# Performance work log

Measured on AMD Instinct MI355X. Metric: run time of the kernel, lower is better.

The kernel has to match this reference:

```python
import jax, jax.numpy as jnp
import numpy as np

N, E, B, K = 100000, 3200000, 500, 30
F_IN, H1, NUM_CLASSES = 128, 64, 18


def _gcn_conv(x, W, b, row, col, w_edge, n_nodes):
    # PyG GCNConv: remove_self_loops happened outside (w_edge=0 on self loops),
    # GCNConv re-adds self loops -> deg = in_deg + 1, norm = d^-1/2[row]*d^-1/2[col].
    xw = x @ W
    deg = jax.ops.segment_sum(w_edge, col, num_segments=n_nodes) + 1.0
    dis = jax.lax.rsqrt(deg)
    coef = dis[row] * dis[col] * w_edge           # [E]
    msg = xw[row] * coef[:, None]                 # [E, C] irregular gather
    agg = jax.ops.segment_sum(msg, col, num_segments=n_nodes)
    agg = agg + xw * (dis * dis)[:, None]         # self-loop term
    return agg + b


def _sort_pool(x, batch, num_graphs, k):
    # SortAggregation: per-graph sort descending by last channel, keep top-k, zero-pad.
    n, c = x.shape
    score = x[:, -1]
    perm = jnp.lexsort((-score, batch))           # sort by (batch asc, score desc)
    b_sorted = batch[perm]
    counts = jax.ops.segment_sum(jnp.ones((n,), x.dtype), batch, num_segments=num_graphs)
    starts = jnp.cumsum(counts) - counts          # segment start offsets
    pos = jnp.arange(n) - starts[b_sorted].astype(jnp.int32)
    pos = jnp.where(pos < k, pos, k)              # out-of-range -> dropped
    out = jnp.zeros((num_graphs, k, c), x.dtype).at[b_sorted, pos].set(x[perm], mode='drop')
    return out.reshape(num_graphs, k * c)


def _conv1d(x, w, b, stride):
    y = jax.lax.conv_general_dilated(x, w, (stride,), 'VALID',
                                     dimension_numbers=('NCH', 'OIH', 'NCH'))
    return y + b[None, :, None]


def setup_inputs() -> dict:
    key = jax.random.key(0)
    ks = jax.random.split(key, 16)
    x = jax.random.normal(ks[0], (N, F_IN), dtype=jnp.float32)
    edge_index = jax.random.randint(ks[1], (2, E), 0, N, dtype=jnp.int32)
    batch = jnp.sort(jax.random.randint(ks[2], (N,), 0, B, dtype=jnp.int32))
    s = 0.05
    return {
        'x': x, 'edge_index': edge_index, 'batch': batch, 'num_graphs': B,
        'W1': jax.random.normal(ks[3], (F_IN, H1), jnp.float32) * s,
        'b1': jnp.zeros((H1,), jnp.float32),
        'W2': jax.random.normal(ks[4], (H1, 1), jnp.float32) * s,
        'b2': jnp.zeros((1,), jnp.float32),
        'conv3_w': jax.random.normal(ks[5], (16, 1, 97), jnp.float32) * s,
        'conv3_b': jnp.zeros((16,), jnp.float32),
        'conv4_w': jax.random.normal(ks[6], (32, 16, 5), jnp.float32) * s,
        'conv4_b': jnp.zeros((32,), jnp.float32),
        'fc1_w': jax.random.normal(ks[7], (192, 128), jnp.float32) * s,
        'fc1_b': jnp.zeros((128,), jnp.float32),
        'fc2_w': jax.random.normal(ks[8], (128, NUM_CLASSES), jnp.float32) * s,
        'fc2_b': jnp.zeros((NUM_CLASSES,), jnp.float32),
    }


def reference(x, edge_index, batch, num_graphs, W1, b1, W2, b2,
              conv3_w, conv3_b, conv4_w, conv4_b, fc1_w, fc1_b, fc2_w, fc2_b):
    row, col = edge_index[0], edge_index[1]
    w_edge = (row != col).astype(x.dtype)         # remove_self_loops
    x1 = jnp.tanh(_gcn_conv(x, W1, b1, row, col, w_edge, x.shape[0]))   # [N,64]
    x2 = jnp.tanh(_gcn_conv(x1, W2, b2, row, col, w_edge, x.shape[0]))  # [N,1]
    xc = jnp.concatenate([x1, x2], axis=-1)       # [N,65]
    p = _sort_pool(xc, batch, num_graphs, K)      # [B, 1950]
    h = p[:, None, :]                             # [B,1,1950]
    h = jax.nn.relu(_conv1d(h, conv3_w, conv3_b, 97))                   # [B,16,20]
    h = jax.lax.reduce_window(h, -jnp.inf, jax.lax.max,
                              (1, 1, 2), (1, 1, 2), 'VALID')            # [B,16,10]
    h = jax.nn.relu(_conv1d(h, conv4_w, conv4_b, 1))                    # [B,32,6]
    h = h.reshape(h.shape[0], -1)                 # [B,192]
    last_layer = jax.nn.relu(h @ fc1_w + fc1_b)   # [B,128] (dropout = eval identity)
    out = last_layer @ fc2_w + fc2_b              # [B,18]
    classes = jax.nn.log_softmax(out, axis=-1)
    return (classes, out, last_layer)
```

## Files before the change

### kernel.cpp

```cpp
#include <hip/hip_runtime.h>
#include <math.h>

#define N_NODES 100000
#define N_EDGES 3200000
#define B_GRAPHS 500
#define K_TOP 30
#define F_INN 128
#define H1C 64
#define NUM_CLASSES 18
#define XC 65
#define P_LEN (K_TOP * XC)
#define C3_OUT 16
#define C3_K 97
#define C3_L 20
#define P2_L 10
#define C4_OUT 32
#define C4_K 5
#define C4_L 6
#define FC1_IN 192
#define FC1_OUT 128

#define BK_SHIFT 7
#define BK_NODES 128
#define NBKT ((N_NODES + BK_NODES - 1) / BK_NODES)
#define BSTRIDE 5120
#define MS_EPT 16
#define MS_EPB (256 * MS_EPT)

typedef __attribute__((ext_vector_type(8))) short bf16x8;
typedef __attribute__((ext_vector_type(4))) float f32x4;

static __device__ __forceinline__ unsigned short f2bf(float f) {
    unsigned int u = __float_as_uint(f);
    u += 0x7FFFu + ((u >> 16) & 1u);
    return (unsigned short)(u >> 16);
}
static __device__ __forceinline__ float bfl(unsigned int u) {
    return __uint_as_float(u << 16);
}
static __device__ __forceinline__ float bfh(unsigned int u) {
    return __uint_as_float(u & 0xFFFF0000u);
}

__global__ __launch_bounds__(256) void k_mscatter(const int* __restrict__ row,
                                                  const int* __restrict__ col,
                                                  int* __restrict__ gcur,
                                                  unsigned int* __restrict__ ebkt) {
    __shared__ int hist[NBKT];
    __shared__ int base[NBKT];
    int tid = threadIdx.x;
    for (int i = tid; i < NBKT; i += 256) hist[i] = 0;
    __syncthreads();
    unsigned int pk[MS_EPT];
    unsigned int pay[MS_EPT];
    int e0 = blockIdx.x * MS_EPB;
#pragma unroll
    for (int j = 0; j < MS_EPT; ++j) {
        int e = e0 + j * 256 + tid;
        pk[j] = 0xFFFFFFFFu;
        if (e < N_EDGES) {
            int r = row[e], c = col[e];
            if (r != c) {
                int b = c >> BK_SHIFT;
                int rank = atomicAdd(&hist[b], 1);
                pk[j] = ((unsigned int)b << 12) | (unsigned int)rank;
                pay[j] = ((unsigned int)r << BK_SHIFT) | (unsigned int)(c & (BK_NODES - 1));
            }
        }
    }
    __syncthreads();
    for (int i = tid; i < NBKT; i += 256)
        base[i] = hist[i] ? (i * BSTRIDE + atomicAdd(&gcur[i], hist[i])) : 0;
    __syncthreads();
#pragma unroll
    for (int j = 0; j < MS_EPT; ++j) {
        if (pk[j] != 0xFFFFFFFFu) {
            int b = pk[j] >> 12;
            int rank = pk[j] & 0xFFF;
            ebkt[base[b] + rank] = pay[j];
        }
    }
}

__global__ __launch_bounds__(256) void k_csr(const unsigned int* __restrict__ ebkt,
                                             const int* __restrict__ gcur,
                                             float* __restrict__ dis,
                                             int2* __restrict__ rowse,
                                             int* __restrict__ erow) {
    __shared__ int cnt[BK_NODES];
    __shared__ int s[256];
    __shared__ int cur[BK_NODES];
    int b = blockIdx.x, t = threadIdx.x;
    if (t < BK_NODES) cnt[t] = 0;
    __syncthreads();
    int lo = b * BSTRIDE;
    int hi = lo + gcur[b];
    for (int i = lo + t; i < hi; i += 256)
        atomicAdd(&cnt[ebkt[i] & (BK_NODES - 1)], 1);
    __syncthreads();
    int v = (t < BK_NODES) ? cnt[t] : 0;
    s[t] = v;
    __syncthreads();
    for (int off = 1; off < BK_NODES; off <<= 1) {
        int add = (t >= off) ? s[t - off] : 0;
        __syncthreads();
        s[t] += add;
        __syncthreads();
    }
    int ex = s[t] - v;
    if (t < BK_NODES) {
        int node = b * BK_NODES + t;
        if (node < N_NODES) {
            dis[node] = rsqrtf((float)v + 1.0f);
            rowse[node] = make_int2(lo + ex, lo + ex + v);
        }
        cur[t] = lo + ex;
    }
    __syncthreads();
    for (int i = lo + t; i < hi; i += 256) {
        unsigned int pk = ebkt[i];
        int cl = pk & (BK_NODES - 1);
        int slot = atomicAdd(&cur[cl], 1);
        erow[slot] = (int)((pk >> BK_SHIFT) << 7);
    }
}

__global__ __launch_bounds__(256) void k_xw1(const float* __restrict__ x,
                                             const float* __restrict__ W1,
                                             const float* __restrict__ dis,
                                             unsigned short* __restrict__ xw) {
    __shared__ unsigned short w1s[16 * 64 * 8];
    int tid = threadIdx.x;
    if (blockIdx.x == 0 && tid < 32)
        ((unsigned int*)(xw + (size_t)N_NODES * H1C))[tid] = 0;
    for (int idx = tid; idx < 16 * 64 * 8; idx += 256) {
        int f = idx >> 9;
        int l = (idx >> 3) & 63;
        int j = idx & 7;
        int kq = f >> 2, t4 = f & 3;
        int k = kq * 32 + ((l >> 4) << 3) + j;
        int n = t4 * 16 + (l & 15);
        w1s[idx] = f2bf(W1[k * H1C + n]);
    }
    __syncthreads();
    int wave = tid >> 6;
    int lane = tid & 63;
    int quad = lane >> 4;
    int m = lane & 15;
    int wrow0 = blockIdx.x * 64 + wave * 16;

    bf16x8 bw[16];
#pragma unroll
    for (int f = 0; f < 16; ++f)
        bw[f] = *(const bf16x8*)&w1s[(f * 64 + lane) * 8];

    f32x4 acc[4];
#pragma unroll
    for (int t = 0; t < 4; ++t) acc[t] = (f32x4){0.f, 0.f, 0.f, 0.f};

    int rowA = wrow0 + m;
    size_t ra = (size_t)(rowA < N_NODES ? rowA : N_NODES - 1);
#pragma unroll
    for (int kq = 0; kq < 4; ++kq) {
        const float* xp = x + ra * F_INN + kq * 32 + quad * 8;
        float4 f0 = ((const float4*)xp)[0];
        float4 f1 = ((const float4*)xp)[1];
        bf16x8 a;
        a[0] = (short)f2bf(f0.x); a[1] = (short)f2bf(f0.y);
        a[2] = (short)f2bf(f0.z); a[3] = (short)f2bf(f0.w);
        a[4] = (short)f2bf(f1.x); a[5] = (short)f2bf(f1.y);
        a[6] = (short)f2bf(f1.z); a[7] = (short)f2bf(f1.w);
#pragma unroll
        for (int t = 0; t < 4; ++t)
            acc[t] = __builtin_amdgcn_mfma_f32_16x16x32_bf16(a, bw[kq * 4 + t], acc[t], 0, 0, 0);
    }
#pragma unroll
    for (int r = 0; r < 4; ++r) {
        int rowD = wrow0 + quad * 4 + r;
        if (rowD < N_NODES) {
            float dsc = dis[rowD];
#pragma unroll
            for (int t = 0; t < 4; ++t)
                xw[(size_t)rowD * H1C + t * 16 + m] = f2bf(acc[t][r] * dsc);
        }
    }
}

__global__ __launch_bounds__(256) void k_agg1f(const int2* __restrict__ rowse,
                                               const int* __restrict__ erow,
                                               const unsigned short* __restrict__ xws,
                                               const float* __restrict__ dis,
                                               const float* __restrict__ b1,
                                               const float* __restrict__ W2,
                                               float* __restrict__ x1,
                                               float* __restrict__ xws2) {
    __shared__ float accs[4][64];
    int tid = threadIdx.x;
    int wave = tid >> 6;
    int lane = tid & 63;
    int wid = blockIdx.x * 4 + wave;
    int grp = lane >> 3;
    int sub = lane & 7;
    int2 se = rowse[wid];
    int base = se.x, endp = se.y;
    const char* xb = (const char*)xws;
    const int ZR = N_NODES << 7;
    float acc[8] = {0.f, 0.f, 0.f, 0.f, 0.f, 0.f, 0.f, 0.f};
    for (int e0 = base; e0 < endp; e0 += 16) {
        int i0 = e0 + grp;
        int i1 = e0 + 8 + grp;
        int o0 = (i0 < endp) ? erow[i0] : ZR;
        int o1 = (i1 < endp) ? erow[i1] : ZR;
        uint4 a = ((const uint4*)(xb + o0))[sub];
        uint4 bq = ((const uint4*)(xb + o1))[sub];
        acc[0] += bfl(a.x) + bfl(bq.x);
        acc[1] += bfh(a.x) + bfh(bq.x);
        acc[2] += bfl(a.y) + bfl(bq.y);
        acc[3] += bfh(a.y) + bfh(bq.y);
        acc[4] += bfl(a.z) + bfl(bq.z);
        acc[5] += bfh(a.z) + bfh(bq.z);
        acc[6] += bfl(a.w) + bfl(bq.w);
        acc[7] += bfh(a.w) + bfh(bq.w);
    }
#pragma unroll
    for (int i = 0; i < 8; ++i) {
        acc[i] += __shfl_xor(acc[i], 8);
        acc[i] += __shfl_xor(acc[i], 16);
        acc[i] += __shfl_xor(acc[i], 32);
    }
    if (grp == 0) {
#pragma unroll
        for (int i = 0; i < 8; ++i) accs[wave][sub * 8 + i] = acc[i];
    }
    __syncthreads();
    float d = dis[wid];
    unsigned int su = xws[(size_t)wid * H1C + lane];
    float self = __uint_as_float(su << 16);
    float v = tanhf(d * (accs[wave][lane] + self) + b1[lane]);
    x1[(size_t)wid * H1C + lane] = v;
    float s = v * W2[lane];
#pragma unroll
    for (int off = 1; off < 64; off <<= 1) s += __shfl_xor(s, off);
    if (lane == 0) xws2[wid] = d * s;
}

__global__ __launch_bounds__(256) void k_x2(const int2* __restrict__ rowse,
                                            const int* __restrict__ erow,
                                            const float* __restrict__ xws2,
                                            const float* __restrict__ dis,
                                            const float* __restrict__ b2,
                                            float* __restrict__ x2) {
    int lane = threadIdx.x & 63;
    int wglob = (blockIdx.x * 256 + threadIdx.x) >> 6;
    int grp = lane >> 3;
    int sub = lane & 7;
    int node = wglob * 8 + grp;
    int2 se = rowse[node];
    float acc = 0.0f;
    for (int i = se.x + sub; i < se.y; i += 8)
        acc += xws2[erow[i] >> 7];
    acc += __shfl_xor(acc, 1);
    acc += __shfl_xor(acc, 2);
    acc += __shfl_xor(acc, 4);
    if (sub == 0)
        x2[node] = tanhf(dis[node] * (acc + xws2[node]) + b2[0]);
}

__global__ __launch_bounds__(256) void k_poolhead(const int* __restrict__ batch,
                                                  const float* __restrict__ x1,
                                                  const float* __restrict__ x2,
                                                  const float* __restrict__ w3, const float* __restrict__ b3,
                                                  const float* __restrict__ w4, const float* __restrict__ b4,
                                                  const float* __restrict__ fw1, const float* __restrict__ fb1,
                                                  const float* __restrict__ fw2, const float* __restrict__ fb2,
                                                  float* __restrict__ out) {
    __shared__ float x2s[512];
    __shared__ int sel[K_TOP];
    __shared__ float ps[P_LEN];
    __shared__ float h1s[C3_OUT * C3_L];
    __shared__ float h2s[C3_OUT * P2_L];
    __shared__ float h3s[FC1_IN];
    __shared__ float lls[FC1_OUT];
    __shared__ float outs[NUM_CLASSES];
    int g = blockIdx.x, tid = threadIdx.x;
    int lo = 0, hi = N_NODES;
    while (lo < hi) { int m = (lo + hi) >> 1; if (batch[m] < g) lo = m + 1; else hi = m; }
    int start = lo;
    hi = N_NODES;
    while (lo < hi) { int m = (lo + hi) >> 1; if (batch[m] < g + 1) lo = m + 1; else hi = m; }
    int end = lo;
    int count = end - start;
    if (count > 512) count = 512;
    for (int t = tid; t < count; t += 256) x2s[t] = x2[start + t];
    __syncthreads();
    int wave = tid >> 6, lane = tid & 63;
    if (wave == 0) {
        unsigned long long k[8];
#pragma unroll
        for (int i = 0; i < 8; ++i) {
            int idx = i * 64 + lane;
            unsigned long long key = 0ULL;
            if (idx < count) {
                unsigned int bits = __float_as_uint(x2s[idx]);
                unsigned int u = (bits & 0x80000000u) ? ~bits : (bits | 0x80000000u);
                key = ((unsigned long long)u << 32) | (unsigned int)(~(unsigned int)(start + idx));
            }
            k[i] = key;
        }
        int kk = count < K_TOP ? count : K_TOP;
        for (int j = 0; j < kk; ++j) {
            unsigned long long best = k[0];
#pragma unroll
            for (int i = 1; i < 8; ++i) if (k[i] > best) best = k[i];
#pragma unroll
            for (int off = 32; off; off >>= 1) {
                unsigned long long o = __shfl_xor(best, off);
                if (o > best) best = o;
            }
            int node = (int)(~(unsigned int)(best & 0xFFFFFFFFULL));
#pragma unroll
            for (int i = 0; i < 8; ++i) if (k[i] == best) k[i] = 0ULL;
            if (lane == 0) sel[j] = node;
        }
        if (lane >= kk && lane < K_TOP) sel[lane] = -1;
    }
    __syncthreads();
    for (int t = tid; t < P_LEN; t += 256) {
        int j = t / XC, c = t - j * XC;
        int node = sel[j];
        float v = 0.0f;
        if (node >= 0) v = (c < H1C) ? x1[(size_t)node * H1C + c] : x2s[node - start];
        ps[t] = v;
    }
    __syncthreads();
    for (int o = tid; o < C3_OUT * C3_L; o += 256) {
        int oc = o / C3_L, pos = o % C3_L;
        float s = b3[oc];
        const float* w = w3 + oc * C3_K;
        int base = pos * C3_K;
        for (int k = 0; k < C3_K; ++k) s += ps[base + k] * w[k];
        h1s[o] = fmaxf(s, 0.0f);
    }
    __syncthreads();
    if (tid < C3_OUT * P2_L) {
        int oc = tid / P2_L, pos = tid % P2_L;
        h2s[tid] = fmaxf(h1s[oc * C3_L + 2 * pos], h1s[oc * C3_L + 2 * pos + 1]);
    }
    __syncthreads();
    if (tid < C4_OUT * C4_L) {
        int oc = tid / C4_L, pos = tid % C4_L;
        float s = b4[oc];
        for (int ic = 0; ic < C3_OUT; ++ic)
#pragma unroll
            for (int k = 0; k < C4_K; ++k)
                s += h2s[ic * P2_L + pos + k] * w4[oc * C3_OUT * C4_K + ic * C4_K + k];
        h3s[oc * C4_L + pos] = fmaxf(s, 0.0f);
    }
    __syncthreads();
    if (tid < FC1_OUT) {
        float s = fb1[tid];
        for (int i = 0; i < FC1_IN; ++i) s += h3s[i] * fw1[i * FC1_OUT + tid];
        float v = fmaxf(s, 0.0f);
        lls[tid] = v;
        out[2 * B_GRAPHS * NUM_CLASSES + (size_t)g * FC1_OUT + tid] = v;
    }
    __syncthreads();
    if (tid < NUM_CLASSES) {
        float s = fb2[tid];
        for (int j = 0; j < FC1_OUT; ++j) s += lls[j] * fw2[j * NUM_CLASSES + tid];
        outs[tid] = s;
        out[B_GRAPHS * NUM_CLASSES + (size_t)g * NUM_CLASSES + tid] = s;
    }
    __syncthreads();
    if (tid < NUM_CLASSES) {
        float m = -INFINITY;
        for (int k2 = 0; k2 < NUM_CLASSES; ++k2) m = fmaxf(m, outs[k2]);
        float se = 0.0f;
        for (int k2 = 0; k2 < NUM_CLASSES; ++k2) se += expf(outs[k2] - m);
        out[(size_t)g * NUM_CLASSES + tid] = outs[tid] - m - logf(se);
    }
}

extern "C" void kernel_launch(void* const* d_in, const int* in_sizes, int n_in,
                              void* d_out, int out_size, void* d_ws, size_t ws_size,
                              hipStream_t stream) {
    const float* x   = (const float*)d_in[0];
    const int*   ei  = (const int*)d_in[1];
    const int*   row = ei;
    const int*   col = ei + N_EDGES;
    const int*   bat = (const int*)d_in[2];
    const float* W1  = (const float*)d_in[4];
    const float* b1  = (const float*)d_in[5];
    const float* W2  = (const float*)d_in[6];
    const float* b2  = (const float*)d_in[7];
    const float* w3  = (const float*)d_in[8];
    const float* b3  = (const float*)d_in[9];
    const float* w4  = (const float*)d_in[10];
    const float* b4  = (const float*)d_in[11];
    const float* fw1 = (const float*)d_in[12];
    const float* fb1 = (const float*)d_in[13];
    const float* fw2 = (const float*)d_in[14];
    const float* fb2 = (const float*)d_in[15];

    char* wsb = (char*)d_ws;
    unsigned short* xws = (unsigned short*)wsb;       wsb += (size_t)(N_NODES + 1) * H1C * 2;
    float* x1     = (float*)wsb;                      wsb += (size_t)N_NODES * H1C * 4;
    int*   erow   = (int*)wsb;                        wsb += (size_t)NBKT * BSTRIDE * 4;
    unsigned int* ebkt = (unsigned int*)x1;
    int*   gcur   = (int*)wsb;                        wsb += (size_t)NBKT * 4;
    int2*  rowse  = (int2*)wsb;                       wsb += (size_t)N_NODES * 8;
    float* dis    = (float*)wsb;                      wsb += (size_t)N_NODES * 4;
    float* xws2   = (float*)wsb;                      wsb += (size_t)N_NODES * 4;
    float* x2     = (float*)wsb;                      wsb += (size_t)N_NODES * 4;
    float* outp   = (float*)d_out;

    hipMemsetAsync(gcur, 0, (size_t)NBKT * 4, stream);

    k_mscatter<<<(N_EDGES + MS_EPB - 1) / MS_EPB, 256, 0, stream>>>(row, col, gcur, ebkt);
    k_csr<<<NBKT, 256, 0, stream>>>(ebkt, gcur, dis, rowse, erow);
    k_xw1<<<(N_NODES + 63) / 64, 256, 0, stream>>>(x, W1, dis, xws);
    k_agg1f<<<N_NODES / 4, 256, 0, stream>>>(rowse, erow, xws, dis, b1, W2, x1, xws2);
    k_x2<<<N_NODES / (8 * 4), 256, 0, stream>>>(rowse, erow, xws2, dis, b2, x2);
    k_poolhead<<<B_GRAPHS, 256, 0, stream>>>(bat, x1, x2,
                                             w3, b3, w4, b4, fw1, fb1, fw2, fb2, outp);
}
```

Measured before the change: 334.8 us.

## Build CSR with global per-node atomics and prefetch first 64 neighbors

Replaces the two-pass bucketed scatter plus per-bucket local CSR build with three kernels. The first counts in-degree per node with global atomics, the second computes per-node offsets inside fixed bucket strides, and the third scatters row indices straight into CSR slots through global atomic cursors. This drops the intermediate bucket array and its second pass, at the cost of many global atomics that contend on random destination nodes. The layer-1 aggregation now loads the first 64 neighbor offsets with one coalesced read, shuffles them across lanes and issues 8 independent gathers up front to raise memory-level parallelism. Edges beyond 64 fall back to a loop.

```diff
diff --git a/kernel.cpp b/kernel.cpp
--- a/kernel.cpp
+++ b/kernel.cpp
@@ -24,8 +24,6 @@
 #define BK_NODES 128
 #define NBKT ((N_NODES + BK_NODES - 1) / BK_NODES)
 #define BSTRIDE 5120
-#define MS_EPT 16
-#define MS_EPB (256 * MS_EPT)
 
 typedef __attribute__((ext_vector_type(8))) short bf16x8;
 typedef __attribute__((ext_vector_type(4))) float f32x4;
@@ -42,63 +40,26 @@
     return __uint_as_float(u & 0xFFFF0000u);
 }
 
-__global__ __launch_bounds__(256) void k_mscatter(const int* __restrict__ row,
-                                                  const int* __restrict__ col,
-                                                  int* __restrict__ gcur,
-                                                  unsigned int* __restrict__ ebkt) {
-    __shared__ int hist[NBKT];
-    __shared__ int base[NBKT];
-    int tid = threadIdx.x;
-    for (int i = tid; i < NBKT; i += 256) hist[i] = 0;
-    __syncthreads();
-    unsigned int pk[MS_EPT];
-    unsigned int pay[MS_EPT];
-    int e0 = blockIdx.x * MS_EPB;
-#pragma unroll
-    for (int j = 0; j < MS_EPT; ++j) {
-        int e = e0 + j * 256 + tid;
-        pk[j] = 0xFFFFFFFFu;
-        if (e < N_EDGES) {
-            int r = row[e], c = col[e];
-            if (r != c) {
-                int b = c >> BK_SHIFT;
-                int rank = atomicAdd(&hist[b], 1);
-                pk[j] = ((unsigned int)b << 12) | (unsigned int)rank;
-                pay[j] = ((unsigned int)r << BK_SHIFT) | (unsigned int)(c & (BK_NODES - 1));
-            }
-        }
-    }
-    __syncthreads();
-    for (int i = tid; i < NBKT; i += 256)
-        base[i] = hist[i] ? (i * BSTRIDE + atomicAdd(&gcur[i], hist[i])) : 0;
-    __syncthreads();
-#pragma unroll
-    for (int j = 0; j < MS_EPT; ++j) {
-        if (pk[j] != 0xFFFFFFFFu) {
-            int b = pk[j] >> 12;
-            int rank = pk[j] & 0xFFF;
-            ebkt[base[b] + rank] = pay[j];
-        }
-    }
-}
-
-__global__ __launch_bounds__(256) void k_csr(const unsigned int* __restrict__ ebkt,
-                                             const int* __restrict__ gcur,
-                                             float* __restrict__ dis,
-                                             int2* __restrict__ rowse,
-                                             int* __restrict__ erow) {
-    __shared__ int cnt[BK_NODES];
-    __shared__ int s[256];
-    __shared__ int cur[BK_NODES];
+__global__ __launch_bounds__(256) void k_count(const int* __restrict__ row,
+                                               const int* __restrict__ col,
+                                               int* __restrict__ ncnt) {
+    int t = blockIdx.x * 256 + threadIdx.x;
+    int4 r4 = ((const int4*)row)[t];
+    int4 c4 = ((const int4*)col)[t];
+    if (r4.x != c4.x) atomicAdd(&ncnt[c4.x], 1);
+    if (r4.y != c4.y) atomicAdd(&ncnt[c4.y], 1);
+    if (r4.z != c4.z) atomicAdd(&ncnt[c4.z], 1);
+    if (r4.w != c4.w) atomicAdd(&ncnt[c4.w], 1);
+}
+
+__global__ __launch_bounds__(128) void k_nodebase(const int* __restrict__ ncnt,
+                                                  float* __restrict__ dis,
+                                                  int2* __restrict__ rowse,
+                                                  int* __restrict__ cur) {
+    __shared__ int s[BK_NODES];
     int b = blockIdx.x, t = threadIdx.x;
-    if (t < BK_NODES) cnt[t] = 0;
-    __syncthreads();
-    int lo = b * BSTRIDE;
-    int hi = lo + gcur[b];
-    for (int i = lo + t; i < hi; i += 256)
-        atomicAdd(&cnt[ebkt[i] & (BK_NODES - 1)], 1);
-    __syncthreads();
-    int v = (t < BK_NODES) ? cnt[t] : 0;
+    int node = b * BK_NODES + t;
+    int v = (node < N_NODES) ? ncnt[node] : 0;
     s[t] = v;
     __syncthreads();
     for (int off = 1; off < BK_NODES; off <<= 1) {
@@ -108,21 +69,25 @@
         __syncthreads();
     }
     int ex = s[t] - v;
-    if (t < BK_NODES) {
-        int node = b * BK_NODES + t;
-        if (node < N_NODES) {
-            dis[node] = rsqrtf((float)v + 1.0f);
-            rowse[node] = make_int2(lo + ex, lo + ex + v);
-        }
-        cur[t] = lo + ex;
-    }
-    __syncthreads();
-    for (int i = lo + t; i < hi; i += 256) {
-        unsigned int pk = ebkt[i];
-        int cl = pk & (BK_NODES - 1);
-        int slot = atomicAdd(&cur[cl], 1);
-        erow[slot] = (int)((pk >> BK_SHIFT) << 7);
-    }
+    if (node < N_NODES) {
+        int base = b * BSTRIDE + ex;
+        dis[node] = rsqrtf((float)v + 1.0f);
+        rowse[node] = make_int2(base, base + v);
+        cur[node] = base;
+    }
+}
+
+__global__ __launch_bounds__(256) void k_scatter2(const int* __restrict__ row,
+                                                  const int* __restrict__ col,
+                                                  int* __restrict__ cur,
+                                                  int* __restrict__ erow) {
+    int t = blockIdx.x * 256 + threadIdx.x;
+    int4 r4 = ((const int4*)row)[t];
+    int4 c4 = ((const int4*)col)[t];
+    if (r4.x != c4.x) { int s = atomicAdd(&cur[c4.x], 1); erow[s] = r4.x << BK_SHIFT; }
+    if (r4.y != c4.y) { int s = atomicAdd(&cur[c4.y], 1); erow[s] = r4.y << BK_SHIFT; }
+    if (r4.z != c4.z) { int s = atomicAdd(&cur[c4.z], 1); erow[s] = r4.z << BK_SHIFT; }
+    if (r4.w != c4.w) { int s = atomicAdd(&cur[c4.w], 1); erow[s] = r4.w << BK_SHIFT; }
 }
 
 __global__ __launch_bounds__(256) void k_xw1(const float* __restrict__ x,
@@ -203,24 +168,40 @@
     int sub = lane & 7;
     int2 se = rowse[wid];
     int base = se.x, endp = se.y;
+    int nE = endp - base;
     const char* xb = (const char*)xws;
     const int ZR = N_NODES << 7;
+
+    int myoff = (lane < nE) ? erow[base + lane] : ZR;
+
+    uint4 a[8];
+#pragma unroll
+    for (int k = 0; k < 8; ++k) {
+        int o = __shfl(myoff, (k << 3) + grp);
+        a[k] = ((const uint4*)(xb + o))[sub];
+    }
     float acc[8] = {0.f, 0.f, 0.f, 0.f, 0.f, 0.f, 0.f, 0.f};
-    for (int e0 = base; e0 < endp; e0 += 16) {
-        int i0 = e0 + grp;
-        int i1 = e0 + 8 + grp;
-        int o0 = (i0 < endp) ? erow[i0] : ZR;
-        int o1 = (i1 < endp) ? erow[i1] : ZR;
-        uint4 a = ((const uint4*)(xb + o0))[sub];
-        uint4 bq = ((const uint4*)(xb + o1))[sub];
-        acc[0] += bfl(a.x) + bfl(bq.x);
-        acc[1] += bfh(a.x) + bfh(bq.x);
-        acc[2] += bfl(a.y) + bfl(bq.y);
-        acc[3] += bfh(a.y) + bfh(bq.y);
-        acc[4] += bfl(a.z) + bfl(bq.z);
-        acc[5] += bfh(a.z) + bfh(bq.z);
-        acc[6] += bfl(a.w) + bfl(bq.w);
-        acc[7] += bfh(a.w) + bfh(bq.w);
+#pragma unroll
+    for (int k = 0; k < 8; ++k) {
+        acc[0] += bfl(a[k].x);
+        acc[1] += bfh(a[k].x);
+        acc[2] += bfl(a[k].y);
+        acc[3] += bfh(a[k].y);
+        acc[4] += bfl(a[k].z);
+        acc[5] += bfh(a[k].z);
+        acc[6] += bfl(a[k].w);
+        acc[7] += bfh(a[k].w);
+    }
+    if (nE > 64) {
+        for (int e0 = base + 64; e0 < endp; e0 += 8) {
+            int i = e0 + grp;
+            int o = (i < endp) ? erow[i] : ZR;
+            uint4 q = ((const uint4*)(xb + o))[sub];
+            acc[0] += bfl(q.x); acc[1] += bfh(q.x);
+            acc[2] += bfl(q.y); acc[3] += bfh(q.y);
+            acc[4] += bfl(q.z); acc[5] += bfh(q.z);
+            acc[6] += bfl(q.w); acc[7] += bfh(q.w);
+        }
     }
 #pragma unroll
     for (int i = 0; i < 8; ++i) {
@@ -406,18 +387,19 @@
     unsigned short* xws = (unsigned short*)wsb;       wsb += (size_t)(N_NODES + 1) * H1C * 2;
     float* x1     = (float*)wsb;                      wsb += (size_t)N_NODES * H1C * 4;
     int*   erow   = (int*)wsb;                        wsb += (size_t)NBKT * BSTRIDE * 4;
-    unsigned int* ebkt = (unsigned int*)x1;
-    int*   gcur   = (int*)wsb;                        wsb += (size_t)NBKT * 4;
     int2*  rowse  = (int2*)wsb;                       wsb += (size_t)N_NODES * 8;
     float* dis    = (float*)wsb;                      wsb += (size_t)N_NODES * 4;
     float* xws2   = (float*)wsb;                      wsb += (size_t)N_NODES * 4;
     float* x2     = (float*)wsb;                      wsb += (size_t)N_NODES * 4;
-    float* outp   = (float*)d_out;
-
-    hipMemsetAsync(gcur, 0, (size_t)NBKT * 4, stream);
-
-    k_mscatter<<<(N_EDGES + MS_EPB - 1) / MS_EPB, 256, 0, stream>>>(row, col, gcur, ebkt);
-    k_csr<<<NBKT, 256, 0, stream>>>(ebkt, gcur, dis, rowse, erow);
+    int* ncnt = (int*)x1;
+    int* cur  = ncnt + N_NODES;
+    float* outp = (float*)d_out;
+
+    hipMemsetAsync(ncnt, 0, (size_t)N_NODES * 4, stream);
+
+    k_count<<<N_EDGES / 1024, 256, 0, stream>>>(row, col, ncnt);
+    k_nodebase<<<NBKT, 128, 0, stream>>>(ncnt, dis, rowse, cur);
+    k_scatter2<<<N_EDGES / 1024, 256, 0, stream>>>(row, col, cur, erow);
     k_xw1<<<(N_NODES + 63) / 64, 256, 0, stream>>>(x, W1, dis, xws);
     k_agg1f<<<N_NODES / 4, 256, 0, stream>>>(rowse, erow, xws, dis, b1, W2, x1, xws2);
     k_x2<<<N_NODES / (8 * 4), 256, 0, stream>>>(rowse, erow, xws2, dis, b2, x2);
```

After: 679.6 us. 2.03x slower.

## Sum gathered neighbor rows with MFMA via LDS transpose reads

Applied to the files above, without the earlier changes.

The per-node neighbor aggregation in the first GCN layer no longer accumulates bf16 values with scalar adds and shuffle reductions. Each wave stages gathered neighbor rows into LDS, reads them back transposed with ds_read_b64_tr_b16, and sums them by multiplying with an all-ones bf16 matrix on MFMA. This moves the accumulation to the matrix cores and drops the cross-lane reduction and block-wide barrier. In exchange it adds LDS round trips and explicit waitcnt stalls per 32 edges, and pads partial chunks with zero-row loads; the gather latency still dominates.

```diff
diff --git a/kernel.cpp b/kernel.cpp
--- a/kernel.cpp
+++ b/kernel.cpp
@@ -27,19 +27,16 @@
 #define MS_EPT 16
 #define MS_EPB (256 * MS_EPT)
 
+#define REG_B 544
+
 typedef __attribute__((ext_vector_type(8))) short bf16x8;
 typedef __attribute__((ext_vector_type(4))) float f32x4;
+typedef __attribute__((ext_vector_type(2))) unsigned int u32x2;
 
 static __device__ __forceinline__ unsigned short f2bf(float f) {
     unsigned int u = __float_as_uint(f);
     u += 0x7FFFu + ((u >> 16) & 1u);
     return (unsigned short)(u >> 16);
-}
-static __device__ __forceinline__ float bfl(unsigned int u) {
-    return __uint_as_float(u << 16);
-}
-static __device__ __forceinline__ float bfh(unsigned int u) {
-    return __uint_as_float(u & 0xFFFF0000u);
 }
 
 __global__ __launch_bounds__(256) void k_mscatter(const int* __restrict__ row,
@@ -186,7 +183,7 @@
     }
 }
 
-__global__ __launch_bounds__(256) void k_agg1f(const int2* __restrict__ rowse,
+__global__ __launch_bounds__(256) void k_agg1m(const int2* __restrict__ rowse,
                                                const int* __restrict__ erow,
                                                const unsigned short* __restrict__ xws,
                                                const float* __restrict__ dis,
@@ -194,7 +191,7 @@
                                                const float* __restrict__ W2,
                                                float* __restrict__ x1,
                                                float* __restrict__ xws2) {
-    __shared__ float accs[4][64];
+    __shared__ __align__(16) char slds[4][8 * REG_B];
     int tid = threadIdx.x;
     int wave = tid >> 6;
     int lane = tid & 63;
@@ -203,40 +200,70 @@
     int sub = lane & 7;
     int2 se = rowse[wid];
     int base = se.x, endp = se.y;
+    int nE = endp - base;
     const char* xb = (const char*)xws;
     const int ZR = N_NODES << 7;
-    float acc[8] = {0.f, 0.f, 0.f, 0.f, 0.f, 0.f, 0.f, 0.f};
-    for (int e0 = base; e0 < endp; e0 += 16) {
-        int i0 = e0 + grp;
-        int i1 = e0 + 8 + grp;
-        int o0 = (i0 < endp) ? erow[i0] : ZR;
-        int o1 = (i1 < endp) ? erow[i1] : ZR;
-        uint4 a = ((const uint4*)(xb + o0))[sub];
-        uint4 bq = ((const uint4*)(xb + o1))[sub];
-        acc[0] += bfl(a.x) + bfl(bq.x);
-        acc[1] += bfh(a.x) + bfh(bq.x);
-        acc[2] += bfl(a.y) + bfl(bq.y);
-        acc[3] += bfh(a.y) + bfh(bq.y);
-        acc[4] += bfl(a.z) + bfl(bq.z);
-        acc[5] += bfh(a.z) + bfh(bq.z);
-        acc[6] += bfl(a.w) + bfl(bq.w);
-        acc[7] += bfh(a.w) + bfh(bq.w);
-    }
-#pragma unroll
-    for (int i = 0; i < 8; ++i) {
-        acc[i] += __shfl_xor(acc[i], 8);
-        acc[i] += __shfl_xor(acc[i], 16);
-        acc[i] += __shfl_xor(acc[i], 32);
-    }
-    if (grp == 0) {
-#pragma unroll
-        for (int i = 0; i < 8; ++i) accs[wave][sub * 8 + i] = acc[i];
-    }
-    __syncthreads();
+
+    char* wreg = &slds[wave][0];
+    char* dst0 = wreg + ((sub >> 1) * 2 + ((grp >> 2) & 1)) * REG_B + (grp & 3) * 32 + (sub & 1) * 16;
+    unsigned int trb = (unsigned int)(size_t)wreg +
+                       (unsigned int)(((lane >> 4) * 64 + (lane & 15)) * 2);
+
+    bf16x8 aones;
+#pragma unroll
+    for (int i = 0; i < 8; ++i) aones[i] = (short)0x3F80;
+
+    f32x4 ac0 = (f32x4){0.f, 0.f, 0.f, 0.f};
+    f32x4 ac1 = ac0, ac2 = ac0, ac3 = ac0;
+
+    for (int w0 = 0; w0 < nE; w0 += 64) {
+        int idx = base + w0 + lane;
+        int myoff = (idx < endp) ? erow[idx] : ZR;
+#pragma unroll
+        for (int hf = 0; hf < 2; ++hf) {
+            if (w0 + hf * 32 < nE) {
+#pragma unroll
+                for (int ii = 0; ii < 4; ++ii) {
+                    int o = __shfl(myoff, hf * 32 + ii * 8 + grp);
+                    uint4 v = ((const uint4*)(xb + o))[sub];
+                    *(uint4*)(dst0 + ii * 128) = v;
+                }
+                asm volatile("s_waitcnt lgkmcnt(0)" ::: "memory");
+                __builtin_amdgcn_sched_barrier(0);
+                u32x2 q0, q1, q2, q3, q4, q5, q6, q7;
+                asm volatile("ds_read_b64_tr_b16 %0, %1 offset:0"    : "=v"(q0) : "v"(trb) : "memory");
+                asm volatile("ds_read_b64_tr_b16 %0, %1 offset:544"  : "=v"(q1) : "v"(trb) : "memory");
+                asm volatile("ds_read_b64_tr_b16 %0, %1 offset:1088" : "=v"(q2) : "v"(trb) : "memory");
+                asm volatile("ds_read_b64_tr_b16 %0, %1 offset:1632" : "=v"(q3) : "v"(trb) : "memory");
+                asm volatile("ds_read_b64_tr_b16 %0, %1 offset:2176" : "=v"(q4) : "v"(trb) : "memory");
+                asm volatile("ds_read_b64_tr_b16 %0, %1 offset:2720" : "=v"(q5) : "v"(trb) : "memory");
+                asm volatile("ds_read_b64_tr_b16 %0, %1 offset:3264" : "=v"(q6) : "v"(trb) : "memory");
+                asm volatile("ds_read_b64_tr_b16 %0, %1 offset:3808" : "=v"(q7) : "v"(trb) : "memory");
+                asm volatile("s_waitcnt lgkmcnt(0)" ::: "memory");
+                __builtin_amdgcn_sched_barrier(0);
+                union FU { bf16x8 f; unsigned int d[4]; };
+                FU f0, f1, f2, f3;
+                f0.d[0] = q0.x; f0.d[1] = q0.y; f0.d[2] = q1.x; f0.d[3] = q1.y;
+                f1.d[0] = q2.x; f1.d[1] = q2.y; f1.d[2] = q3.x; f1.d[3] = q3.y;
+                f2.d[0] = q4.x; f2.d[1] = q4.y; f2.d[2] = q5.x; f2.d[3] = q5.y;
+                f3.d[0] = q6.x; f3.d[1] = q6.y; f3.d[2] = q7.x; f3.d[3] = q7.y;
+                ac0 = __builtin_amdgcn_mfma_f32_16x16x32_bf16(aones, f0.f, ac0, 0, 0, 0);
+                ac1 = __builtin_amdgcn_mfma_f32_16x16x32_bf16(aones, f1.f, ac1, 0, 0, 0);
+                ac2 = __builtin_amdgcn_mfma_f32_16x16x32_bf16(aones, f2.f, ac2, 0, 0, 0);
+                ac3 = __builtin_amdgcn_mfma_f32_16x16x32_bf16(aones, f3.f, ac3, 0, 0, 0);
+            }
+        }
+    }
+    float v0 = __shfl(ac0[0], lane & 15);
+    float v1 = __shfl(ac1[0], lane & 15);
+    float v2 = __shfl(ac2[0], lane & 15);
+    float v3 = __shfl(ac3[0], lane & 15);
+    int ts = lane >> 4;
+    float aggv = ts == 0 ? v0 : (ts == 1 ? v1 : (ts == 2 ? v2 : v3));
     float d = dis[wid];
     unsigned int su = xws[(size_t)wid * H1C + lane];
     float self = __uint_as_float(su << 16);
-    float v = tanhf(d * (accs[wave][lane] + self) + b1[lane]);
+    float v = tanhf(d * (aggv + self) + b1[lane]);
     x1[(size_t)wid * H1C + lane] = v;
     float s = v * W2[lane];
 #pragma unroll
@@ -419,7 +446,7 @@
     k_mscatter<<<(N_EDGES + MS_EPB - 1) / MS_EPB, 256, 0, stream>>>(row, col, gcur, ebkt);
     k_csr<<<NBKT, 256, 0, stream>>>(ebkt, gcur, dis, rowse, erow);
     k_xw1<<<(N_NODES + 63) / 64, 256, 0, stream>>>(x, W1, dis, xws);
-    k_agg1f<<<N_NODES / 4, 256, 0, stream>>>(rowse, erow, xws, dis, b1, W2, x1, xws2);
+    k_agg1m<<<N_NODES / 4, 256, 0, stream>>>(rowse, erow, xws, dis, b1, W2, x1, xws2);
     k_x2<<<N_NODES / (8 * 4), 256, 0, stream>>>(rowse, erow, xws2, dis, b2, x2);
     k_poolhead<<<B_GRAPHS, 256, 0, stream>>>(bat, x1, x2,
                                              w3, b3, w4, b4, fw1, fb1, fw2, fb2, outp);
```

Measured after the change: 322.7 us. -3.6%, faster.
